# Kernel optimization log

Hardware: AMD Instinct MI355X
Metric: run time of the kernel (lower is better)

## Reference

```python
import jax, jax.numpy as jnp
import numpy as np

P = 3          # graph partitions
CO = 64        # out_channels
KS = 9         # temporal kernel size (Gamma)
STRIDE = 1     # temporal stride
EPS = 1e-3     # keras BatchNormalization default epsilon


def setup_inputs() -> dict:
    key = jax.random.key(0)
    k1, k2, k3 = jax.random.split(key, 3)
    x = jax.random.normal(k1, (32, 64, 300, 25), dtype=jnp.float32)      # (N, C_in, L, V)
    A = jax.random.uniform(k2, (3, 25, 25), dtype=jnp.float32)           # (P, V, V)
    W = jax.random.normal(k3, (64, 192), dtype=jnp.float32) * 0.05       # (C_in, C_out*P)
    gamma = jnp.ones((64,), dtype=jnp.float32)
    beta = jnp.zeros((64,), dtype=jnp.float32)
    mean = jnp.zeros((64,), dtype=jnp.float32)
    var = jnp.ones((64,), dtype=jnp.float32)
    return {"x": x, "A": A, "W": W, "gamma": gamma, "beta": beta, "mean": mean, "var": var}


def _lt_matrix(L):
    # sum of shifted identities: lt[r, r + i*STRIDE] = 1 for i in [0, KS//STRIDE)
    lt = jnp.zeros((L, L), dtype=jnp.float32)
    for i in range(KS // STRIDE):
        lt = lt + jnp.eye(L, k=i * STRIDE, dtype=jnp.float32)
    return lt


def reference(x, A, W, gamma, beta, mean, var):
    N, C, L, V = x.shape
    res = x  # identity residual (in_channels == out_channels, stride == 1)
    # 1x1 conv: (N,C,L,V) x (C, CO*P) -> (N, CO*P, L, V); channel k = c*P + p (split into CO groups of P)
    y = jnp.einsum('nclv,ck->nklv', x, W)
    y = y.reshape(N, CO, P, L, V)  # (N, C_out, P, L, V)
    # partitioned graph matmul over joints: contract V with A[p]
    z = jnp.einsum('ncplv,pvw->ncplw', y, A)
    # temporal aggregation via handcrafted banded matrix, then sum over partitions
    lt = _lt_matrix(L)
    t = jnp.einsum('ncplv,lm->ncmv', z, lt)  # partition sum fused into einsum
    # BN (inference) over channel axis + ReLU
    inv = gamma / jnp.sqrt(var + EPS)
    xn = (t - mean[None, :, None, None]) * inv[None, :, None, None] + beta[None, :, None, None]
    xn = jax.nn.relu(xn)
    # residual add + final ReLU (dropout is identity at inference)
    return jax.nn.relu(xn + res)
```

## Files before the change

kernel.cpp:

```cpp
#include <hip/hip_runtime.h>
#include <cstdint>
#include <cstddef>

typedef short bf16x8 __attribute__((ext_vector_type(8)));
typedef float f32x4 __attribute__((ext_vector_type(4)));

#define EPS 1e-3f

__device__ __forceinline__ short f32_to_bf16s(float f) {
    union { float f; uint32_t u; } v; v.f = f;
    return (short)((v.u + 0x7FFFu + ((v.u >> 16) & 1u)) >> 16);
}

__global__ __launch_bounds__(256) void prep_kernel(const float* __restrict__ A,
                                                   const float* __restrict__ W,
                                                   unsigned short* __restrict__ wt,
                                                   unsigned short* __restrict__ at) {
    int idx = blockIdx.x * 256 + threadIdx.x;
    if (idx < 12288) {
        int kp = idx >> 6, ci = idx & 63;
        wt[idx] = (unsigned short)f32_to_bf16s(W[ci * 192 + kp]);
    } else {
        int j = idx - 12288;
        if (j < 3072) {
            int w = j / 96, k = j - w * 96;
            float val = 0.f;
            if (w < 25 && k < 75) {
                int p = k / 25, v = k - p * 25;
                val = A[(p * 25 + v) * 25 + w];
            }
            at[j] = (unsigned short)f32_to_bf16s(val);
        }
    }
}

__global__ __launch_bounds__(512, 4) void mega_kernel(
    const float* __restrict__ x,
    const unsigned short* __restrict__ wt,
    const unsigned short* __restrict__ at,
    const float* __restrict__ gamma, const float* __restrict__ beta,
    const float* __restrict__ mean, const float* __restrict__ var,
    float* __restrict__ out) {
    const int ch = blockIdx.x, n = blockIdx.y;
    const int l0 = ch * 8;
    const int tid = threadIdx.x;
    const int wv = tid >> 6, lane = tid & 63, q = lane >> 4, lcol = lane & 15;

    __shared__ __align__(16) short smem[13312];
    __shared__ float scs[64], shs[64];

    bf16x8 b2[2][3];
    #pragma unroll
    for (int nt = 0; nt < 2; ++nt)
        #pragma unroll
        for (int s = 0; s < 3; ++s)
            b2[nt][s] = *(const bf16x8*)(at + (size_t)(nt * 16 + lcol) * 96 + 32 * s + 8 * q);
    if (tid < 64) {
        float sc = gamma[tid] * rsqrtf(var[tid] + EPS);
        scs[tid] = sc;
        shs[tid] = beta[tid] - mean[tid] * sc;
    }

    #pragma unroll 1
    for (int rep = 0; rep < 4; ++rep) {
        int cidx = tid + rep * 512;
        if (cidx < 1600) {
            int ci = cidx / 25, v = cidx - ci * 25;
            const float* xp = x + (size_t)(n * 64 + ci) * 7500 + v;
            float vals[16];
            #pragma unroll
            for (int i = 0; i < 16; ++i) {
                int l = l0 - 8 + i;
                vals[i] = (l >= 0 && l < 300) ? xp[l * 25] : 0.f;
            }
            float run = vals[0] + vals[1] + vals[2] + vals[3]
                      + vals[4] + vals[5] + vals[6] + vals[7];
            short* wb = &smem[(ci >> 3) * 1656 + (ci & 7)];
            #pragma unroll
            for (int j = 0; j < 8; ++j) {
                run += vals[j + 8];
                wb[(j * 25 + v) * 8] = f32_to_bf16s(run);
                run -= vals[j];
            }
        }
    }
    __syncthreads();

    bf16x8 b1[2][2];
    #pragma unroll
    for (int nt = 0; nt < 2; ++nt) {
        int col = wv * 25 + nt * 16 + lcol;
        #pragma unroll
        for (int s = 0; s < 2; ++s)
            b1[nt][s] = *(const bf16x8*)&smem[(4 * s + q) * 1656 + col * 8];
    }
    __syncthreads();

    #pragma unroll
    for (int i = lane; i < 512; i += 64) {
        int r = i >> 5, cc = 72 + (i & 31);
        smem[(wv * 16 + r) * 104 + cc] = 0;
    }

    const int lg = l0 + wv;
    const size_t outrow = ((size_t)n * 64 * 300 + lg) * 25;

    #pragma unroll 1
    for (int g = 0; g < 4; ++g) {
        bf16x8 a1[3][2];
        #pragma unroll
        for (int mt = 0; mt < 3; ++mt)
            #pragma unroll
            for (int s = 0; s < 2; ++s)
                a1[mt][s] = *(const bf16x8*)(wt + (size_t)(g * 48 + mt * 16 + lcol) * 64 + 32 * s + 8 * q);

        f32x4 acc[3][2];
        #pragma unroll
        for (int mt = 0; mt < 3; ++mt)
            #pragma unroll
            for (int nt = 0; nt < 2; ++nt) acc[mt][nt] = (f32x4){0.f, 0.f, 0.f, 0.f};
        #pragma unroll
        for (int s = 0; s < 2; ++s)
            #pragma unroll
            for (int mt = 0; mt < 3; ++mt) {
                bf16x8 av = a1[mt][s];
                #pragma unroll
                for (int nt = 0; nt < 2; ++nt)
                    acc[mt][nt] = __builtin_amdgcn_mfma_f32_16x16x32_bf16(av, b1[nt][s], acc[mt][nt], 0, 0, 0);
            }

        float res[2][4];
        #pragma unroll
        for (int nt = 0; nt < 2; ++nt) {
            int w = nt * 16 + lcol;
            bool val = (w < 25) && (lg < 300);
            #pragma unroll
            for (int r = 0; r < 4; ++r) {
                int c = g * 16 + 4 * q + r;
                res[nt][r] = val ? x[outrow + (size_t)c * 7500 + w] : 0.f;
            }
        }

        #pragma unroll
        for (int mt = 0; mt < 3; ++mt)
            #pragma unroll
            for (int nt = 0; nt < 2; ++nt) {
                int v = nt * 16 + lcol;
                if (v < 25) {
                    #pragma unroll
                    for (int r = 0; r < 4; ++r) {
                        int kpl = mt * 16 + 4 * q + r;
                        int cl = kpl / 3, p = kpl - 3 * cl;
                        smem[(wv * 16 + cl) * 104 + 25 * p + v] = f32_to_bf16s(acc[mt][nt][r]);
                    }
                }
            }

        f32x4 c0 = {0.f, 0.f, 0.f, 0.f}, c1 = {0.f, 0.f, 0.f, 0.f};
        #pragma unroll
        for (int s = 0; s < 3; ++s) {
            bf16x8 a2 = *(const bf16x8*)&smem[(wv * 16 + lcol) * 104 + 32 * s + 8 * q];
            c0 = __builtin_amdgcn_mfma_f32_16x16x32_bf16(a2, b2[0][s], c0, 0, 0, 0);
            c1 = __builtin_amdgcn_mfma_f32_16x16x32_bf16(a2, b2[1][s], c1, 0, 0, 0);
        }

        if (lg < 300) {
            #pragma unroll
            for (int nt = 0; nt < 2; ++nt) {
                int w = nt * 16 + lcol;
                if (w < 25) {
                    f32x4 cc = nt ? c1 : c0;
                    #pragma unroll
                    for (int r = 0; r < 4; ++r) {
                        int c = g * 16 + 4 * q + r;
                        float o = fmaxf(cc[r] * scs[c] + shs[c], 0.f);
                        out[outrow + (size_t)c * 7500 + w] = fmaxf(o + res[nt][r], 0.f);
                    }
                }
            }
        }
    }
}

extern "C" void kernel_launch(void* const* d_in, const int* in_sizes, int n_in,
                              void* d_out, int out_size, void* d_ws, size_t ws_size,
                              hipStream_t stream) {
    const float* x     = (const float*)d_in[0];
    const float* A     = (const float*)d_in[1];
    const float* W     = (const float*)d_in[2];
    const float* gamma = (const float*)d_in[3];
    const float* beta  = (const float*)d_in[4];
    const float* mean  = (const float*)d_in[5];
    const float* var   = (const float*)d_in[6];
    float* out = (float*)d_out;

    char* ws = (char*)d_ws;
    unsigned short* wt = (unsigned short*)ws;
    unsigned short* at = (unsigned short*)(ws + 24576);

    prep_kernel<<<60, 256, 0, stream>>>(A, W, wt, at);
    mega_kernel<<<dim3(38, 32), 512, 0, stream>>>(x, wt, at, gamma, beta, mean, var, out);
}
```

Measured before the change: 164.5 us.

## Process two batch items per block and prefetch next item's input during compute

Each block now handles two batch samples, halving the grid. While the four channel groups of the first sample are computed, global loads and bf16 packing of the windowed temporal sums for the second sample are issued and held in registers. They are written to shared memory once the first sample is finished. This is meant to hide global-load latency behind MFMA work, at the cost of more registers and fewer blocks (608), which may reduce occupancy and parallelism.

```diff
diff --git a/kernel.cpp b/kernel.cpp
--- a/kernel.cpp
+++ b/kernel.cpp
@@ -34,6 +34,122 @@
     }
 }
 
+__device__ __forceinline__ void p1_issue(const float* __restrict__ xn, int l0, int cidx,
+                                         bool act, float* v16) {
+    int ci = cidx / 25, v = cidx - ci * 25;
+    const float* xp = xn + (size_t)ci * 7500 + v;
+    #pragma unroll
+    for (int i = 0; i < 16; ++i) {
+        int l = l0 - 8 + i;
+        v16[i] = (act && l >= 0 && l < 300) ? xp[l * 25] : 0.f;
+    }
+}
+
+__device__ __forceinline__ void p1_pack(const float* v16, uint32_t* pk) {
+    float run = v16[0] + v16[1] + v16[2] + v16[3] + v16[4] + v16[5] + v16[6] + v16[7];
+    #pragma unroll
+    for (int jj = 0; jj < 4; ++jj) {
+        run += v16[2 * jj + 8];
+        uint32_t lo = (uint32_t)(unsigned short)f32_to_bf16s(run);
+        run -= v16[2 * jj];
+        run += v16[2 * jj + 9];
+        uint32_t hi = (uint32_t)(unsigned short)f32_to_bf16s(run);
+        run -= v16[2 * jj + 1];
+        pk[jj] = lo | (hi << 16);
+    }
+}
+
+__device__ __forceinline__ void p1_write(short* smem, int cidx, const uint32_t* pk) {
+    int ci = cidx / 25, v = cidx - ci * 25;
+    short* wb = &smem[(ci >> 3) * 1656 + (ci & 7) + v * 8];
+    #pragma unroll
+    for (int jj = 0; jj < 4; ++jj) {
+        wb[(2 * jj) * 200]     = (short)(pk[jj] & 0xFFFF);
+        wb[(2 * jj + 1) * 200] = (short)(pk[jj] >> 16);
+    }
+}
+
+__device__ __forceinline__ void do_group(int g, const unsigned short* __restrict__ wt,
+    short* smem, const bf16x8 (&b1)[2][2], const bf16x8 (&b2)[2][3],
+    const float* __restrict__ xn, float* __restrict__ outn,
+    const float* scs, const float* shs,
+    int lg, int wv, int q, int lcol)
+{
+    bf16x8 a1[3][2];
+    #pragma unroll
+    for (int mt = 0; mt < 3; ++mt)
+        #pragma unroll
+        for (int s = 0; s < 2; ++s)
+            a1[mt][s] = *(const bf16x8*)(wt + (size_t)(g * 48 + mt * 16 + lcol) * 64 + 32 * s + 8 * q);
+
+    f32x4 acc[3][2];
+    #pragma unroll
+    for (int mt = 0; mt < 3; ++mt)
+        #pragma unroll
+        for (int nt = 0; nt < 2; ++nt) acc[mt][nt] = (f32x4){0.f, 0.f, 0.f, 0.f};
+    #pragma unroll
+    for (int s = 0; s < 2; ++s)
+        #pragma unroll
+        for (int mt = 0; mt < 3; ++mt) {
+            bf16x8 av = a1[mt][s];
+            #pragma unroll
+            for (int nt = 0; nt < 2; ++nt)
+                acc[mt][nt] = __builtin_amdgcn_mfma_f32_16x16x32_bf16(av, b1[nt][s], acc[mt][nt], 0, 0, 0);
+        }
+
+    const size_t rbase = (size_t)lg * 25;
+    float res[2][4];
+    #pragma unroll
+    for (int nt = 0; nt < 2; ++nt) {
+        int w = nt * 16 + lcol;
+        bool val = (w < 25) && (lg < 300);
+        #pragma unroll
+        for (int r = 0; r < 4; ++r) {
+            int c = g * 16 + 4 * q + r;
+            res[nt][r] = val ? xn[rbase + (size_t)c * 7500 + w] : 0.f;
+        }
+    }
+
+    #pragma unroll
+    for (int mt = 0; mt < 3; ++mt)
+        #pragma unroll
+        for (int nt = 0; nt < 2; ++nt) {
+            int v = nt * 16 + lcol;
+            if (v < 25) {
+                #pragma unroll
+                for (int r = 0; r < 4; ++r) {
+                    int kpl = mt * 16 + 4 * q + r;
+                    int cl = kpl / 3, p = kpl - 3 * cl;
+                    smem[(wv * 16 + cl) * 104 + 25 * p + v] = f32_to_bf16s(acc[mt][nt][r]);
+                }
+            }
+        }
+
+    f32x4 c0 = {0.f, 0.f, 0.f, 0.f}, c1 = {0.f, 0.f, 0.f, 0.f};
+    #pragma unroll
+    for (int s = 0; s < 3; ++s) {
+        bf16x8 a2 = *(const bf16x8*)&smem[(wv * 16 + lcol) * 104 + 32 * s + 8 * q];
+        c0 = __builtin_amdgcn_mfma_f32_16x16x32_bf16(a2, b2[0][s], c0, 0, 0, 0);
+        c1 = __builtin_amdgcn_mfma_f32_16x16x32_bf16(a2, b2[1][s], c1, 0, 0, 0);
+    }
+
+    if (lg < 300) {
+        #pragma unroll
+        for (int nt = 0; nt < 2; ++nt) {
+            int w = nt * 16 + lcol;
+            if (w < 25) {
+                f32x4 cc = nt ? c1 : c0;
+                #pragma unroll
+                for (int r = 0; r < 4; ++r) {
+                    int c = g * 16 + 4 * q + r;
+                    float o = fmaxf(cc[r] * scs[c] + shs[c], 0.f);
+                    outn[rbase + (size_t)c * 7500 + w] = fmaxf(o + res[nt][r], 0.f);
+                }
+            }
+        }
+    }
+}
+
 __global__ __launch_bounds__(512, 4) void mega_kernel(
     const float* __restrict__ x,
     const unsigned short* __restrict__ wt,
@@ -41,13 +157,19 @@
     const float* __restrict__ gamma, const float* __restrict__ beta,
     const float* __restrict__ mean, const float* __restrict__ var,
     float* __restrict__ out) {
-    const int ch = blockIdx.x, n = blockIdx.y;
+    const int ch = blockIdx.x;
+    const int n0 = blockIdx.y * 2;
     const int l0 = ch * 8;
     const int tid = threadIdx.x;
     const int wv = tid >> 6, lane = tid & 63, q = lane >> 4, lcol = lane & 15;
 
     __shared__ __align__(16) short smem[13312];
     __shared__ float scs[64], shs[64];
+
+    const float* xn0 = x + (size_t)n0 * 480000;
+    const float* xn1 = xn0 + 480000;
+    float* outn0 = out + (size_t)n0 * 480000;
+    float* outn1 = outn0 + 480000;
 
     bf16x8 b2[2][3];
     #pragma unroll
@@ -64,26 +186,17 @@
     #pragma unroll 1
     for (int rep = 0; rep < 4; ++rep) {
         int cidx = tid + rep * 512;
-        if (cidx < 1600) {
-            int ci = cidx / 25, v = cidx - ci * 25;
-            const float* xp = x + (size_t)(n * 64 + ci) * 7500 + v;
-            float vals[16];
-            #pragma unroll
-            for (int i = 0; i < 16; ++i) {
-                int l = l0 - 8 + i;
-                vals[i] = (l >= 0 && l < 300) ? xp[l * 25] : 0.f;
-            }
-            float run = vals[0] + vals[1] + vals[2] + vals[3]
-                      + vals[4] + vals[5] + vals[6] + vals[7];
-            short* wb = &smem[(ci >> 3) * 1656 + (ci & 7)];
-            #pragma unroll
-            for (int j = 0; j < 8; ++j) {
-                run += vals[j + 8];
-                wb[(j * 25 + v) * 8] = f32_to_bf16s(run);
-                run -= vals[j];
-            }
-        }
-    }
+        bool act = cidx < 1600;
+        float t16[16]; uint32_t tpk[4];
+        p1_issue(xn0, l0, cidx, act, t16);
+        p1_pack(t16, tpk);
+        if (act) p1_write(smem, cidx, tpk);
+    }
+
+    float v16[16];
+    uint32_t pk0[4], pk1[4], pk2[4], pk3[4];
+    p1_issue(xn1, l0, tid, true, v16);
+
     __syncthreads();
 
     bf16x8 b1[2][2];
@@ -103,83 +216,46 @@
     }
 
     const int lg = l0 + wv;
-    const size_t outrow = ((size_t)n * 64 * 300 + lg) * 25;
+
+    do_group(0, wt, smem, b1, b2, xn0, outn0, scs, shs, lg, wv, q, lcol);
+    p1_pack(v16, pk0);
+    p1_issue(xn1, l0, tid + 512, true, v16);
+    do_group(1, wt, smem, b1, b2, xn0, outn0, scs, shs, lg, wv, q, lcol);
+    p1_pack(v16, pk1);
+    p1_issue(xn1, l0, tid + 1024, true, v16);
+    do_group(2, wt, smem, b1, b2, xn0, outn0, scs, shs, lg, wv, q, lcol);
+    p1_pack(v16, pk2);
+    p1_issue(xn1, l0, tid + 1536, tid < 64, v16);
+    do_group(3, wt, smem, b1, b2, xn0, outn0, scs, shs, lg, wv, q, lcol);
+    p1_pack(v16, pk3);
+
+    __syncthreads();
+
+    p1_write(smem, tid, pk0);
+    p1_write(smem, tid + 512, pk1);
+    p1_write(smem, tid + 1024, pk2);
+    if (tid < 64) p1_write(smem, tid + 1536, pk3);
+
+    __syncthreads();
+
+    #pragma unroll
+    for (int nt = 0; nt < 2; ++nt) {
+        int col = wv * 25 + nt * 16 + lcol;
+        #pragma unroll
+        for (int s = 0; s < 2; ++s)
+            b1[nt][s] = *(const bf16x8*)&smem[(4 * s + q) * 1656 + col * 8];
+    }
+    __syncthreads();
+
+    #pragma unroll
+    for (int i = lane; i < 512; i += 64) {
+        int r = i >> 5, cc = 72 + (i & 31);
+        smem[(wv * 16 + r) * 104 + cc] = 0;
+    }
 
     #pragma unroll 1
-    for (int g = 0; g < 4; ++g) {
-        bf16x8 a1[3][2];
-        #pragma unroll
-        for (int mt = 0; mt < 3; ++mt)
-            #pragma unroll
-            for (int s = 0; s < 2; ++s)
-                a1[mt][s] = *(const bf16x8*)(wt + (size_t)(g * 48 + mt * 16 + lcol) * 64 + 32 * s + 8 * q);
-
-        f32x4 acc[3][2];
-        #pragma unroll
-        for (int mt = 0; mt < 3; ++mt)
-            #pragma unroll
-            for (int nt = 0; nt < 2; ++nt) acc[mt][nt] = (f32x4){0.f, 0.f, 0.f, 0.f};
-        #pragma unroll
-        for (int s = 0; s < 2; ++s)
-            #pragma unroll
-            for (int mt = 0; mt < 3; ++mt) {
-                bf16x8 av = a1[mt][s];
-                #pragma unroll
-                for (int nt = 0; nt < 2; ++nt)
-                    acc[mt][nt] = __builtin_amdgcn_mfma_f32_16x16x32_bf16(av, b1[nt][s], acc[mt][nt], 0, 0, 0);
-            }
-
-        float res[2][4];
-        #pragma unroll
-        for (int nt = 0; nt < 2; ++nt) {
-            int w = nt * 16 + lcol;
-            bool val = (w < 25) && (lg < 300);
-            #pragma unroll
-            for (int r = 0; r < 4; ++r) {
-                int c = g * 16 + 4 * q + r;
-                res[nt][r] = val ? x[outrow + (size_t)c * 7500 + w] : 0.f;
-            }
-        }
-
-        #pragma unroll
-        for (int mt = 0; mt < 3; ++mt)
-            #pragma unroll
-            for (int nt = 0; nt < 2; ++nt) {
-                int v = nt * 16 + lcol;
-                if (v < 25) {
-                    #pragma unroll
-                    for (int r = 0; r < 4; ++r) {
-                        int kpl = mt * 16 + 4 * q + r;
-                        int cl = kpl / 3, p = kpl - 3 * cl;
-                        smem[(wv * 16 + cl) * 104 + 25 * p + v] = f32_to_bf16s(acc[mt][nt][r]);
-                    }
-                }
-            }
-
-        f32x4 c0 = {0.f, 0.f, 0.f, 0.f}, c1 = {0.f, 0.f, 0.f, 0.f};
-        #pragma unroll
-        for (int s = 0; s < 3; ++s) {
-            bf16x8 a2 = *(const bf16x8*)&smem[(wv * 16 + lcol) * 104 + 32 * s + 8 * q];
-            c0 = __builtin_amdgcn_mfma_f32_16x16x32_bf16(a2, b2[0][s], c0, 0, 0, 0);
-            c1 = __builtin_amdgcn_mfma_f32_16x16x32_bf16(a2, b2[1][s], c1, 0, 0, 0);
-        }
-
-        if (lg < 300) {
-            #pragma unroll
-            for (int nt = 0; nt < 2; ++nt) {
-                int w = nt * 16 + lcol;
-                if (w < 25) {
-                    f32x4 cc = nt ? c1 : c0;
-                    #pragma unroll
-                    for (int r = 0; r < 4; ++r) {
-                        int c = g * 16 + 4 * q + r;
-                        float o = fmaxf(cc[r] * scs[c] + shs[c], 0.f);
-                        out[outrow + (size_t)c * 7500 + w] = fmaxf(o + res[nt][r], 0.f);
-                    }
-                }
-            }
-        }
-    }
+    for (int g = 0; g < 4; ++g)
+        do_group(g, wt, smem, b1, b2, xn1, outn1, scs, shs, lg, wv, q, lcol);
 }
 
 extern "C" void kernel_launch(void* const* d_in, const int* in_sizes, int n_in,
@@ -199,5 +275,5 @@
     unsigned short* at = (unsigned short*)(ws + 24576);
 
     prep_kernel<<<60, 256, 0, stream>>>(A, W, wt, at);
-    mega_kernel<<<dim3(38, 32), 512, 0, stream>>>(x, wt, at, gamma, beta, mean, var, out);
-}
+    mega_kernel<<<dim3(38, 16), 512, 0, stream>>>(x, wt, at, gamma, beta, mean, var, out);
+}
```

Result: slower. 212.7 us (+29.3%).

## Process two samples per block with XCD-aware block remapping and nontemporal stores

Applied to the files above, without the earlier changes.

Each block now handles two batch samples in sequence, which halves the grid and spreads the per-block setup (loading the A fragments and the BN scale/shift) over twice the work. The linear block index is remapped so that consecutive time chunks of the same samples are grouped, likely to land on the same XCD and share halo reads of x in L2. Output stores become nontemporal to avoid polluting the cache. The risks are lower occupancy or parallelism (608 blocks instead of 1216) and a serial dependence between the two samples inside a block.

```diff
diff --git a/kernel.cpp b/kernel.cpp
--- a/kernel.cpp
+++ b/kernel.cpp
@@ -34,39 +34,101 @@
     }
 }
 
-__global__ __launch_bounds__(512, 4) void mega_kernel(
-    const float* __restrict__ x,
+__device__ __forceinline__ void do_group(int g, const unsigned short* __restrict__ wt,
+    short* smem, const bf16x8 (&b1)[2][2], const bf16x8 (&b2)[2][3],
+    const float* __restrict__ xn, float* __restrict__ outn,
+    const float* scs, const float* shs,
+    int lg, int wv, int q, int lcol)
+{
+    bf16x8 a1[3][2];
+    #pragma unroll
+    for (int mt = 0; mt < 3; ++mt)
+        #pragma unroll
+        for (int s = 0; s < 2; ++s)
+            a1[mt][s] = *(const bf16x8*)(wt + (size_t)(g * 48 + mt * 16 + lcol) * 64 + 32 * s + 8 * q);
+
+    f32x4 acc[3][2];
+    #pragma unroll
+    for (int mt = 0; mt < 3; ++mt)
+        #pragma unroll
+        for (int nt = 0; nt < 2; ++nt) acc[mt][nt] = (f32x4){0.f, 0.f, 0.f, 0.f};
+    #pragma unroll
+    for (int s = 0; s < 2; ++s)
+        #pragma unroll
+        for (int mt = 0; mt < 3; ++mt) {
+            bf16x8 av = a1[mt][s];
+            #pragma unroll
+            for (int nt = 0; nt < 2; ++nt)
+                acc[mt][nt] = __builtin_amdgcn_mfma_f32_16x16x32_bf16(av, b1[nt][s], acc[mt][nt], 0, 0, 0);
+        }
+
+    const size_t rbase = (size_t)lg * 25;
+    float res[2][4];
+    #pragma unroll
+    for (int nt = 0; nt < 2; ++nt) {
+        int w = nt * 16 + lcol;
+        bool val = (w < 25) && (lg < 300);
+        #pragma unroll
+        for (int r = 0; r < 4; ++r) {
+            int c = g * 16 + 4 * q + r;
+            res[nt][r] = val ? xn[rbase + (size_t)c * 7500 + w] : 0.f;
+        }
+    }
+
+    #pragma unroll
+    for (int mt = 0; mt < 3; ++mt)
+        #pragma unroll
+        for (int nt = 0; nt < 2; ++nt) {
+            int v = nt * 16 + lcol;
+            if (v < 25) {
+                #pragma unroll
+                for (int r = 0; r < 4; ++r) {
+                    int kpl = mt * 16 + 4 * q + r;
+                    int cl = kpl / 3, p = kpl - 3 * cl;
+                    smem[(wv * 16 + cl) * 104 + 25 * p + v] = f32_to_bf16s(acc[mt][nt][r]);
+                }
+            }
+        }
+
+    f32x4 c0 = {0.f, 0.f, 0.f, 0.f}, c1 = {0.f, 0.f, 0.f, 0.f};
+    #pragma unroll
+    for (int s = 0; s < 3; ++s) {
+        bf16x8 a2 = *(const bf16x8*)&smem[(wv * 16 + lcol) * 104 + 32 * s + 8 * q];
+        c0 = __builtin_amdgcn_mfma_f32_16x16x32_bf16(a2, b2[0][s], c0, 0, 0, 0);
+        c1 = __builtin_amdgcn_mfma_f32_16x16x32_bf16(a2, b2[1][s], c1, 0, 0, 0);
+    }
+
+    if (lg < 300) {
+        #pragma unroll
+        for (int nt = 0; nt < 2; ++nt) {
+            int w = nt * 16 + lcol;
+            if (w < 25) {
+                f32x4 cc = nt ? c1 : c0;
+                #pragma unroll
+                for (int r = 0; r < 4; ++r) {
+                    int c = g * 16 + 4 * q + r;
+                    float o = fmaxf(cc[r] * scs[c] + shs[c], 0.f);
+                    __builtin_nontemporal_store(fmaxf(o + res[nt][r], 0.f),
+                                                &outn[rbase + (size_t)c * 7500 + w]);
+                }
+            }
+        }
+    }
+}
+
+__device__ __forceinline__ void process_sample(
+    const float* __restrict__ xn, float* __restrict__ outn,
     const unsigned short* __restrict__ wt,
-    const unsigned short* __restrict__ at,
-    const float* __restrict__ gamma, const float* __restrict__ beta,
-    const float* __restrict__ mean, const float* __restrict__ var,
-    float* __restrict__ out) {
-    const int ch = blockIdx.x, n = blockIdx.y;
-    const int l0 = ch * 8;
-    const int tid = threadIdx.x;
-    const int wv = tid >> 6, lane = tid & 63, q = lane >> 4, lcol = lane & 15;
-
-    __shared__ __align__(16) short smem[13312];
-    __shared__ float scs[64], shs[64];
-
-    bf16x8 b2[2][3];
-    #pragma unroll
-    for (int nt = 0; nt < 2; ++nt)
-        #pragma unroll
-        for (int s = 0; s < 3; ++s)
-            b2[nt][s] = *(const bf16x8*)(at + (size_t)(nt * 16 + lcol) * 96 + 32 * s + 8 * q);
-    if (tid < 64) {
-        float sc = gamma[tid] * rsqrtf(var[tid] + EPS);
-        scs[tid] = sc;
-        shs[tid] = beta[tid] - mean[tid] * sc;
-    }
-
+    short* smem, const bf16x8 (&b2)[2][3],
+    const float* scs, const float* shs,
+    int l0, int tid, int wv, int lane, int q, int lcol)
+{
     #pragma unroll 1
     for (int rep = 0; rep < 4; ++rep) {
         int cidx = tid + rep * 512;
         if (cidx < 1600) {
             int ci = cidx / 25, v = cidx - ci * 25;
-            const float* xp = x + (size_t)(n * 64 + ci) * 7500 + v;
+            const float* xp = xn + (size_t)ci * 7500 + v;
             float vals[16];
             #pragma unroll
             for (int i = 0; i < 16; ++i) {
@@ -103,83 +165,49 @@
     }
 
     const int lg = l0 + wv;
-    const size_t outrow = ((size_t)n * 64 * 300 + lg) * 25;
-
     #pragma unroll 1
-    for (int g = 0; g < 4; ++g) {
-        bf16x8 a1[3][2];
-        #pragma unroll
-        for (int mt = 0; mt < 3; ++mt)
-            #pragma unroll
-            for (int s = 0; s < 2; ++s)
-                a1[mt][s] = *(const bf16x8*)(wt + (size_t)(g * 48 + mt * 16 + lcol) * 64 + 32 * s + 8 * q);
-
-        f32x4 acc[3][2];
-        #pragma unroll
-        for (int mt = 0; mt < 3; ++mt)
-            #pragma unroll
-            for (int nt = 0; nt < 2; ++nt) acc[mt][nt] = (f32x4){0.f, 0.f, 0.f, 0.f};
-        #pragma unroll
-        for (int s = 0; s < 2; ++s)
-            #pragma unroll
-            for (int mt = 0; mt < 3; ++mt) {
-                bf16x8 av = a1[mt][s];
-                #pragma unroll
-                for (int nt = 0; nt < 2; ++nt)
-                    acc[mt][nt] = __builtin_amdgcn_mfma_f32_16x16x32_bf16(av, b1[nt][s], acc[mt][nt], 0, 0, 0);
-            }
-
-        float res[2][4];
-        #pragma unroll
-        for (int nt = 0; nt < 2; ++nt) {
-            int w = nt * 16 + lcol;
-            bool val = (w < 25) && (lg < 300);
-            #pragma unroll
-            for (int r = 0; r < 4; ++r) {
-                int c = g * 16 + 4 * q + r;
-                res[nt][r] = val ? x[outrow + (size_t)c * 7500 + w] : 0.f;
-            }
-        }
-
-        #pragma unroll
-        for (int mt = 0; mt < 3; ++mt)
-            #pragma unroll
-            for (int nt = 0; nt < 2; ++nt) {
-                int v = nt * 16 + lcol;
-                if (v < 25) {
-                    #pragma unroll
-                    for (int r = 0; r < 4; ++r) {
-                        int kpl = mt * 16 + 4 * q + r;
-                        int cl = kpl / 3, p = kpl - 3 * cl;
-                        smem[(wv * 16 + cl) * 104 + 25 * p + v] = f32_to_bf16s(acc[mt][nt][r]);
-                    }
-                }
-            }
-
-        f32x4 c0 = {0.f, 0.f, 0.f, 0.f}, c1 = {0.f, 0.f, 0.f, 0.f};
-        #pragma unroll
-        for (int s = 0; s < 3; ++s) {
-            bf16x8 a2 = *(const bf16x8*)&smem[(wv * 16 + lcol) * 104 + 32 * s + 8 * q];
-            c0 = __builtin_amdgcn_mfma_f32_16x16x32_bf16(a2, b2[0][s], c0, 0, 0, 0);
-            c1 = __builtin_amdgcn_mfma_f32_16x16x32_bf16(a2, b2[1][s], c1, 0, 0, 0);
-        }
-
-        if (lg < 300) {
-            #pragma unroll
-            for (int nt = 0; nt < 2; ++nt) {
-                int w = nt * 16 + lcol;
-                if (w < 25) {
-                    f32x4 cc = nt ? c1 : c0;
-                    #pragma unroll
-                    for (int r = 0; r < 4; ++r) {
-                        int c = g * 16 + 4 * q + r;
-                        float o = fmaxf(cc[r] * scs[c] + shs[c], 0.f);
-                        out[outrow + (size_t)c * 7500 + w] = fmaxf(o + res[nt][r], 0.f);
-                    }
-                }
-            }
-        }
-    }
+    for (int g = 0; g < 4; ++g)
+        do_group(g, wt, smem, b1, b2, xn, outn, scs, shs, lg, wv, q, lcol);
+}
+
+__global__ __launch_bounds__(512, 4) void mega_kernel(
+    const float* __restrict__ x,
+    const unsigned short* __restrict__ wt,
+    const unsigned short* __restrict__ at,
+    const float* __restrict__ gamma, const float* __restrict__ beta,
+    const float* __restrict__ mean, const float* __restrict__ var,
+    float* __restrict__ out) {
+    const int lin = blockIdx.x + 38 * blockIdx.y;
+    const int logical = (lin & 7) * 76 + (lin >> 3);
+    const int ch = logical % 38;
+    const int n0 = (logical / 38) * 2;
+
+    const int l0 = ch * 8;
+    const int tid = threadIdx.x;
+    const int wv = tid >> 6, lane = tid & 63, q = lane >> 4, lcol = lane & 15;
+
+    __shared__ __align__(16) short smem[13312];
+    __shared__ float scs[64], shs[64];
+
+    const float* xn0 = x + (size_t)n0 * 480000;
+    float* outn0 = out + (size_t)n0 * 480000;
+
+    bf16x8 b2[2][3];
+    #pragma unroll
+    for (int nt = 0; nt < 2; ++nt)
+        #pragma unroll
+        for (int s = 0; s < 3; ++s)
+            b2[nt][s] = *(const bf16x8*)(at + (size_t)(nt * 16 + lcol) * 96 + 32 * s + 8 * q);
+    if (tid < 64) {
+        float sc = gamma[tid] * rsqrtf(var[tid] + EPS);
+        scs[tid] = sc;
+        shs[tid] = beta[tid] - mean[tid] * sc;
+    }
+
+    process_sample(xn0, outn0, wt, smem, b2, scs, shs, l0, tid, wv, lane, q, lcol);
+    __syncthreads();
+    process_sample(xn0 + 480000, outn0 + 480000, wt, smem, b2, scs, shs,
+                   l0, tid, wv, lane, q, lcol);
 }
 
 extern "C" void kernel_launch(void* const* d_in, const int* in_sizes, int n_in,
@@ -199,5 +227,5 @@
     unsigned short* at = (unsigned short*)(ws + 24576);
 
     prep_kernel<<<60, 256, 0, stream>>>(A, W, wt, at);
-    mega_kernel<<<dim3(38, 32), 512, 0, stream>>>(x, wt, at, gamma, beta, mean, var, out);
-}
+    mega_kernel<<<dim3(38, 16), 512, 0, stream>>>(x, wt, at, gamma, beta, mean, var, out);
+}
```

Measured after the change: 182.7 us. 11.1% more time.
